# Optimization experiments

Hardware: AMD Instinct MI355X
Metric: run time of the kernel (lower is better)

## Reference

```python
import jax, jax.numpy as jnp
import numpy as np

N = 8192        # particles
NBH = 64        # black holes
L = 46.0        # box side -> ~32 neighbors per particle at radius 4.5
K = 4           # kernel_size per axis
KK = K * K * K
EXTENT = 9.0    # radius_scale(1.5) * 6 * particle_radius(1)
EXTENT_BH = 4.0 * EXTENT
EP = 300000     # padded particle-particle edge count
EB = 160000     # padded bh->particle edge count
CIN = 4         # vel(3) + mass(1)
C0, C1, C2, C3 = 32, 64, 64, 3
FOUR_OVER_PI = 4.0 / np.pi


def _ball_query_np(query, points, radius, cap, pad_seg):
    """Brute-force host-side ball query. Returns padded (src, dst); padding
    uses dst == pad_seg (a sentinel segment that is dropped later)."""
    r2 = radius * radius
    src, dst = [], []
    for i in range(0, query.shape[0], 1024):
        q = query[i:i + 1024]
        d2 = ((q[:, None, :] - points[None, :, :]) ** 2).sum(-1)
        m = (d2 < r2) & (d2 > 0.0)  # radius_search_ignore_query_points
        qi, pj = np.nonzero(m)
        dst.append(qi + i)
        src.append(pj)
    src = np.concatenate(src).astype(np.int32)
    dst = np.concatenate(dst).astype(np.int32)
    n = min(len(src), cap)
    out_s = np.zeros(cap, np.int32)
    out_d = np.full(cap, pad_seg, np.int32)
    out_s[:n] = src[:n]
    out_d[:n] = dst[:n]
    return out_s, out_d


def setup_inputs() -> dict:
    rng = np.random.RandomState(0)
    pos = (rng.rand(N, 3) * L).astype(np.float32)
    vel = rng.randn(N, 3).astype(np.float32)
    mass = rng.rand(N).astype(np.float32)
    bh_pos = (rng.rand(NBH, 3) * L).astype(np.float32)
    bh_vel = rng.randn(NBH, 3).astype(np.float32)
    bh_mass = (rng.rand(NBH) * 10.0).astype(np.float32)
    pp_src, pp_dst = _ball_query_np(pos, pos, EXTENT * 0.5, EP, N)
    bh_src, bh_dst = _ball_query_np(pos, bh_pos, EXTENT_BH * 0.5, EB, N)

    def w(*s):
        return (rng.randn(*s) * 0.05).astype(np.float32)

    inp = dict(
        pos=jnp.asarray(pos), vel=jnp.asarray(vel), mass=jnp.asarray(mass),
        bh_pos=jnp.asarray(bh_pos), bh_vel=jnp.asarray(bh_vel), bh_mass=jnp.asarray(bh_mass),
        pp_src=jnp.asarray(pp_src), pp_dst=jnp.asarray(pp_dst),
        bh_src=jnp.asarray(bh_src), bh_dst=jnp.asarray(bh_dst),
        W0a=jnp.asarray(w(K, K, K, CIN, C0)), b0a=jnp.zeros(C0, jnp.float32),
        Wd0=jnp.asarray(w(CIN, C0)), bd0=jnp.zeros(C0, jnp.float32),
        W0b=jnp.asarray(w(K, K, K, CIN, C0)), b0b=jnp.zeros(C0, jnp.float32),
        W1=jnp.asarray(w(K, K, K, 3 * C0, C1)), b1=jnp.zeros(C1, jnp.float32),
        Wd1=jnp.asarray(w(3 * C0, C1)), bd1=jnp.zeros(C1, jnp.float32),
        W2=jnp.asarray(w(K, K, K, C1, C2)), b2=jnp.zeros(C2, jnp.float32),
        Wd2=jnp.asarray(w(C1, C2)), bd2=jnp.zeros(C2, jnp.float32),
        W3=jnp.asarray(w(K, K, K, C2, C3)), b3=jnp.zeros(C3, jnp.float32),
        Wd3=jnp.asarray(w(C2, C3)), bd3=jnp.zeros(C3, jnp.float32),
    )
    return inp


def _ball_to_cube(p):
    """Volume-preserving map from unit ball to cube [-1,1]^3 (sphere->cylinder->cube)."""
    eps = 1e-8
    x, y, z = p[..., 0], p[..., 1], p[..., 2]
    sq = x * x + y * y + z * z
    nrm = jnp.sqrt(sq)
    xy = x * x + y * y
    # sphere -> cylinder
    caps = 1.25 * z * z > xy
    s_caps = jnp.sqrt(3.0 * nrm / (nrm + jnp.abs(z) + eps))
    s_side = nrm / jnp.sqrt(xy + eps)
    s = jnp.where(caps, s_caps, s_side)
    valid = sq > eps
    cx = jnp.where(valid, x * s, 0.0)
    cy = jnp.where(valid, y * s, 0.0)
    cz = jnp.where(valid, jnp.where(caps, jnp.sign(z) * nrm, 1.5 * z), 0.0)
    # cylinder -> cube (concentric disc-to-square, area preserving)
    rxy = jnp.sqrt(cx * cx + cy * cy)
    regA = cx * cx >= cy * cy
    safe_cx = jnp.where(jnp.abs(cx) > eps, cx, 1.0)
    safe_cy = jnp.where(jnp.abs(cy) > eps, cy, 1.0)
    uA = jnp.sign(cx) * rxy
    vA = uA * FOUR_OVER_PI * jnp.arctan(cy / safe_cx)
    vB = jnp.sign(cy) * rxy
    uB = vB * FOUR_OVER_PI * jnp.arctan(cx / safe_cy)
    okxy = rxy > eps
    u = jnp.where(okxy, jnp.where(regA, uA, uB), 0.0)
    v = jnp.where(okxy, jnp.where(regA, vA, vB), 0.0)
    return jnp.stack([u, v, cz], axis=-1)


def _cconv(feats, pos_src, pos_dst, src, dst, W, b, extent):
    """ContinuousConv: ball-query edges (src->dst), poly6 window, trilinear
    kernel interpolation (align_corners=True), scatter-sum, no normalization."""
    n_out = pos_dst.shape[0]
    radius = 0.5 * extent
    ps = jnp.take(pos_src, src, axis=0)                       # [E,3]
    pd = jnp.take(pos_dst, jnp.minimum(dst, n_out - 1), axis=0)
    d = (ps - pd) * (1.0 / radius)                            # normalized offsets
    r_sqr = jnp.sum(d * d, axis=-1)
    win = jnp.clip((1.0 - r_sqr) ** 3, 0.0, 1.0)              # window_poly6
    u = _ball_to_cube(d)                                      # in [-1,1]^3
    t = (u + 1.0) * (0.5 * (K - 1))                           # align_corners grid coords
    i0f = jnp.clip(jnp.floor(t), 0, K - 2)
    i0 = i0f.astype(jnp.int32)
    f = t - i0f                                               # trilinear fractions
    fe = jnp.take(feats, src, axis=0) * win[:, None]          # [E,Cin]
    Cin = feats.shape[1]
    Wf = W.reshape(KK, Cin, -1)
    T = jnp.zeros(((n_out + 1) * KK, Cin), feats.dtype)
    for dx in (0, 1):
        wx = f[:, 0] if dx else 1.0 - f[:, 0]
        for dy in (0, 1):
            wy = f[:, 1] if dy else 1.0 - f[:, 1]
            for dz in (0, 1):
                wz = f[:, 2] if dz else 1.0 - f[:, 2]
                k = ((i0[:, 0] + dx) * K + (i0[:, 1] + dy)) * K + (i0[:, 2] + dz)
                idx = dst * KK + k                            # sentinel dst==n_out dropped
                T = T + jax.ops.segment_sum((wx * wy * wz)[:, None] * fe, idx,
                                            num_segments=(n_out + 1) * KK)
    T = T.reshape(n_out + 1, KK, Cin)[:n_out]                 # [N,64,Cin]
    return jnp.einsum('nkc,kcd->nd', T, Wf) + b


def _forward(pos, vel, mass, bh_pos, bh_vel, bh_mass,
             W0a, b0a, Wd0, bd0, W0b, b0b, W1, b1, Wd1, bd1,
             W2, b2, Wd2, bd2, W3, b3, Wd3, bd3,
             pp_src, pp_dst, bh_src, bh_dst):
    feats = jnp.concatenate([vel, mass[:, None]], axis=-1)        # [N,4]
    bh_feats = jnp.concatenate([bh_vel, bh_mass[:, None]], axis=-1)
    c0 = _cconv(feats, pos, pos, pp_src, pp_dst, W0a, b0a, EXTENT)      # [N,32]
    d0 = feats @ Wd0 + bd0                                               # [N,32]
    cb = _cconv(bh_feats, bh_pos, pos, bh_src, bh_dst, W0b, b0b, EXTENT_BH)
    h = jnp.concatenate([c0, cb, d0], axis=-1)                           # [N,96]
    c1 = jax.nn.relu(_cconv(h, pos, pos, pp_src, pp_dst, W1, b1, EXTENT))
    d1 = jax.nn.relu(h @ Wd1 + bd1)
    h1 = c1 + d1                                                         # 64 != 96 -> no residual
    c2 = jax.nn.relu(_cconv(h1, pos, pos, pp_src, pp_dst, W2, b2, EXTENT))
    d2 = jax.nn.relu(h1 @ Wd2 + bd2)
    h2 = c2 + d2 + h1                                                    # 64 == 64 -> residual
    c3 = _cconv(h2, pos, pos, pp_src, pp_dst, W3, b3, EXTENT)
    d3 = h2 @ Wd3 + bd3
    return c3 + d3                                                       # accelerations [N,3]


def reference(pos, vel, mass, bh_pos, bh_vel, bh_mass,
              pp_src, pp_dst, bh_src, bh_dst,
              W0a, b0a, Wd0, bd0, W0b, b0b, W1, b1, Wd1, bd1,
              W2, b2, Wd2, bd2, W3, b3, Wd3, bd3):
    return _forward(pos, vel, mass, bh_pos, bh_vel, bh_mass,
                    W0a, b0a, Wd0, bd0, W0b, b0b, W1, b1, Wd1, bd1,
                    W2, b2, Wd2, bd2, W3, b3, Wd3, bd3,
                    pp_src, pp_dst, bh_src, bh_dst)
```

## Files before the change

kernel.cpp:

```cpp
#include <hip/hip_runtime.h>
#include <math.h>

#define NPART 8192
#define NBHX  64
#define EPX   300000
#define EBX   160000
#define FOUR_OVER_PI 1.27323954473516f

typedef __attribute__((ext_vector_type(8))) short bf16x8;
typedef __attribute__((ext_vector_type(4))) float f32x4;

__device__ __forceinline__ float signf(float x){ return (x>0.f)?1.f:((x<0.f)?-1.f:0.f); }
__device__ __forceinline__ unsigned short f2bf(float f){
  unsigned u = __float_as_uint(f);
  u += 0x7FFFu + ((u >> 16) & 1u);
  return (unsigned short)(u >> 16);
}
__device__ __forceinline__ float bf2f(unsigned short h){
  return __uint_as_float(((unsigned)h) << 16);
}
__device__ __forceinline__ float bfl(unsigned u){ return __uint_as_float(u << 16); }
__device__ __forceinline__ float bfh(unsigned u){ return __uint_as_float(u & 0xffff0000u); }

__global__ void feats_kernel(const float* __restrict__ vel, const float* __restrict__ mass,
                             const float* __restrict__ bhvel, const float* __restrict__ bhmass,
                             float* __restrict__ feats, float* __restrict__ bhfeats) {
  int i = blockIdx.x*256 + threadIdx.x;
  if (i < NPART) {
    feats[i*4+0]=vel[i*3+0]; feats[i*4+1]=vel[i*3+1]; feats[i*4+2]=vel[i*3+2]; feats[i*4+3]=mass[i];
  }
  if (i < NBHX) {
    bhfeats[i*4+0]=bhvel[i*3+0]; bhfeats[i*4+1]=bhvel[i*3+1]; bhfeats[i*4+2]=bhvel[i*3+2]; bhfeats[i*4+3]=bhmass[i];
  }
}

__global__ void geom_kernel(const float* __restrict__ ppos, const float* __restrict__ qpos,
                            const int* __restrict__ src, const int* __restrict__ dst,
                            int E, int n_out, float inv_radius,
                            int* __restrict__ gsrc, int* __restrict__ gbase, float* __restrict__ gw) {
  int e = blockIdx.x*256 + threadIdx.x;
  if (e >= E) return;
  int s = src[e], t = dst[e];
  gsrc[e] = s;
  if (t >= n_out) {
    gbase[e] = 0;
    for (int j=0;j<8;j++) gw[(size_t)e*8+j] = 0.f;
    return;
  }
  float x = (ppos[s*3+0] - qpos[t*3+0]) * inv_radius;
  float y = (ppos[s*3+1] - qpos[t*3+1]) * inv_radius;
  float z = (ppos[s*3+2] - qpos[t*3+2]) * inv_radius;
  float r2 = x*x + y*y + z*z;
  float w1 = 1.f - r2;
  float win = fminf(fmaxf(w1*w1*w1, 0.f), 1.f);
  const float eps = 1e-8f;
  float sq = r2;
  float nrm = sqrtf(sq);
  float xy = x*x + y*y;
  bool caps = (1.25f*z*z > xy);
  float s_caps = sqrtf(3.f*nrm/(nrm + fabsf(z) + eps));
  float s_side = nrm / sqrtf(xy + eps);
  float sc = caps ? s_caps : s_side;
  bool valid = sq > eps;
  float cx = valid ? x*sc : 0.f;
  float cy = valid ? y*sc : 0.f;
  float cz = valid ? (caps ? signf(z)*nrm : 1.5f*z) : 0.f;
  float rxy = sqrtf(cx*cx + cy*cy);
  bool regA = (cx*cx >= cy*cy);
  float safe_cx = (fabsf(cx) > eps) ? cx : 1.0f;
  float safe_cy = (fabsf(cy) > eps) ? cy : 1.0f;
  float uA = signf(cx)*rxy;
  float vA = uA * FOUR_OVER_PI * atanf(cy/safe_cx);
  float vB = signf(cy)*rxy;
  float uB = vB * FOUR_OVER_PI * atanf(cx/safe_cy);
  bool okxy = rxy > eps;
  float u = okxy ? (regA ? uA : uB) : 0.f;
  float v = okxy ? (regA ? vA : vB) : 0.f;
  float tt[3] = { (u+1.f)*1.5f, (v+1.f)*1.5f, (cz+1.f)*1.5f };
  int i0[3]; float f[3];
#pragma unroll
  for (int ax=0; ax<3; ax++) {
    float tf = floorf(tt[ax]);
    tf = fminf(fmaxf(tf, 0.f), 2.f);
    i0[ax] = (int)tf;
    f[ax] = tt[ax] - tf;
  }
  gbase[e] = (i0[0]*4 + i0[1])*4 + i0[2];
  float wx0 = 1.f - f[0], wx1 = f[0];
#pragma unroll
  for (int q=0;q<4;q++) {
    float wyz = win * ((q&2) ? f[1] : 1.f - f[1]) * ((q&1) ? f[2] : 1.f - f[2]);
    gw[(size_t)e*8 + q*2 + 0] = wyz * wx0;
    gw[(size_t)e*8 + q*2 + 1] = wyz * wx1;
  }
}

__global__ void csr_kernel(const int* __restrict__ dst, int E, int* __restrict__ rs) {
  int n = blockIdx.x*256 + threadIdx.x;
  if (n > NPART) return;
  int lo = 0, hi = E;
  while (lo < hi) { int mid = (lo+hi)>>1; if (dst[mid] < n) lo = mid+1; else hi = mid; }
  rs[n] = lo;
}

__global__ void zerohist_kernel(int* __restrict__ hist) {
  int i = blockIdx.x*256 + threadIdx.x;
  if (i < 4096) hist[i] = 0;
}
__global__ void cellhist_kernel(const float* __restrict__ pos, int* __restrict__ cell,
                                int* __restrict__ hist) {
  int i = blockIdx.x*256 + threadIdx.x;
  if (i >= NPART) return;
  const float inv = 16.0f/46.0f;
  int ix = min(15, max(0, (int)(pos[i*3+0]*inv)));
  int iy = min(15, max(0, (int)(pos[i*3+1]*inv)));
  int iz = min(15, max(0, (int)(pos[i*3+2]*inv)));
  int c = (ix*16+iy)*16+iz;
  cell[i] = c;
  atomicAdd(&hist[c], 1);
}
__global__ __launch_bounds__(256) void scan_kernel(const int* __restrict__ hist, int* __restrict__ offs) {
  __shared__ int wsum[4];
  int t = threadIdx.x;
  int base = t*16;
  int loc[16]; int s = 0;
#pragma unroll
  for (int i=0;i<16;i++){ loc[i]=s; s+=hist[base+i]; }
  int lane = t & 63, wv = t >> 6;
  int pre = s;
  for (int off=1; off<64; off<<=1) {
    int v = __shfl_up(pre, off);
    if (lane >= off) pre += v;
  }
  if (lane == 63) wsum[wv] = pre;
  __syncthreads();
  int wbase = 0;
  for (int w=0; w<wv; w++) wbase += wsum[w];
  int ex = wbase + pre - s;
#pragma unroll
  for (int i=0;i<16;i++) offs[base+i] = ex + loc[i];
}
__global__ void scatterorder_kernel(const int* __restrict__ cell, int* __restrict__ offs,
                                    int* __restrict__ order) {
  int i = blockIdx.x*256 + threadIdx.x;
  if (i >= NPART) return;
  int p = atomicAdd(&offs[cell[i]], 1);
  order[p] = i;
}

__device__ __forceinline__ int swz_block(int bid, int nb) {
  return (bid & 7)*(nb >> 3) + (bid >> 3);
}

__global__ void wtransY_kernel(const float* __restrict__ W, int KC, int CO, int DP,
                               unsigned short* __restrict__ BT) {
  int idx = blockIdx.x*256 + threadIdx.x;
  int N = 64*DP;
  if (idx >= N*KC) return;
  int n = idx / KC, c = idx - n*KC;
  int k = n / DP, d = n - k*DP;
  float v = (d < CO) ? W[((size_t)k*KC + c)*CO + d] : 0.f;
  BT[idx] = f2bf(v);
}

__global__ void y0_kernel(const float* __restrict__ feats4, const float* __restrict__ W0,
                          int NS, unsigned short* __restrict__ Y0) {
  int idx = blockIdx.x*256 + threadIdx.x;
  if (idx >= NS*256) return;
  int oct = idx & 3, k = (idx>>2) & 63, s = idx >> 8;
  float4 f = *(const float4*)(feats4 + (size_t)s*4);
  const float* w = W0 + (size_t)k*128 + oct*8;
  unsigned short o[8];
#pragma unroll
  for (int i=0;i<8;i++) {
    float v = f.x*w[i] + f.y*w[32+i] + f.z*w[64+i] + f.w*w[96+i];
    o[i] = f2bf(v);
  }
  uint4 u;
  u.x = (unsigned)o[0] | ((unsigned)o[1]<<16);
  u.y = (unsigned)o[2] | ((unsigned)o[3]<<16);
  u.z = (unsigned)o[4] | ((unsigned)o[5]<<16);
  u.w = (unsigned)o[6] | ((unsigned)o[7]<<16);
  *(uint4*)(Y0 + ((size_t)s*64 + k)*32 + oct*8) = u;
}

__global__ __launch_bounds__(256) void gemm_y_kernel(
    const unsigned short* __restrict__ A, const unsigned short* __restrict__ BT,
    int KC, int Ntot, unsigned short* __restrict__ Y) {
  const int wid  = threadIdx.x >> 6;
  const int lane = threadIdx.x & 63;
  const int r = lane & 15, g = lane >> 4;
  const int m0 = blockIdx.x*128 + wid*32;
  const int n0 = blockIdx.y*64;
  f32x4 acc[2][4];
#pragma unroll
  for (int h=0;h<2;h++)
#pragma unroll
    for (int n=0;n<4;n++) acc[h][n] = (f32x4){0.f,0.f,0.f,0.f};
  const unsigned short* A0 = A + (size_t)(m0 + r)*KC;
  const unsigned short* A1 = A + (size_t)(m0 + 16 + r)*KC;
  for (int k0 = 0; k0 < KC; k0 += 32) {
    int ko = k0 + g*8;
    bf16x8 a0 = *(const bf16x8*)(A0 + ko);
    bf16x8 a1 = *(const bf16x8*)(A1 + ko);
#pragma unroll
    for (int n=0; n<4; n++) {
      bf16x8 b = *(const bf16x8*)(BT + (size_t)(n0 + n*16 + r)*KC + ko);
      acc[0][n] = __builtin_amdgcn_mfma_f32_16x16x32_bf16(a0, b, acc[0][n], 0, 0, 0);
      acc[1][n] = __builtin_amdgcn_mfma_f32_16x16x32_bf16(a1, b, acc[1][n], 0, 0, 0);
    }
  }
#pragma unroll
  for (int h=0;h<2;h++)
#pragma unroll
    for (int n=0;n<4;n++)
#pragma unroll
      for (int j=0;j<4;j++)
        Y[(size_t)(m0 + h*16 + g*4 + j)*Ntot + n0 + n*16 + r] = f2bf(acc[h][n][j]);
}

__device__ __forceinline__ void xor_add4(f32x4& a, int mask) {
  a.x += __shfl_xor(a.x, mask);
  a.y += __shfl_xor(a.y, mask);
  a.z += __shfl_xor(a.z, mask);
  a.w += __shfl_xor(a.w, mask);
}

__global__ __launch_bounds__(256) void gather_l0_kernel(
    const int* __restrict__ order,
    const int* __restrict__ rsP, const int* __restrict__ gsP, const int* __restrict__ gbP, const float* __restrict__ gwP,
    const int* __restrict__ rsB, const int* __restrict__ gsB, const int* __restrict__ gbB, const float* __restrict__ gwB,
    const unsigned short* __restrict__ Y0a, const unsigned short* __restrict__ Y0b,
    const float* __restrict__ feats4, const float* __restrict__ Wd0, const float* __restrict__ bd0,
    const float* __restrict__ b0a, const float* __restrict__ b0b,
    float* __restrict__ hf, unsigned short* __restrict__ hb) {
  const int sb = swz_block(blockIdx.x, gridDim.x);
  const int node = order[sb*4 + (threadIdx.x >> 6)];
  const int lane = threadIdx.x & 63;
  const int j = lane >> 3, cg = lane & 7;
  const int koff = ((j&4)<<2) | ((j&2)<<1) | (j&1);
  const int widx = (j&3)*2 + (j>>2);
  f32x4 accP = {0.f,0.f,0.f,0.f}, accB = {0.f,0.f,0.f,0.f};
  {
    int e0 = rsP[node], e1 = rsP[node+1];
    int e = e0;
    for (; e + 4 <= e1; e += 4) {
      uint2 y[4]; float w[4];
#pragma unroll
      for (int i=0;i<4;i++) {
        int s = gsP[e+i], b = gbP[e+i];
        y[i] = *(const uint2*)(Y0a + ((size_t)(s*64 + b + koff))*32 + cg*4);
        w[i] = gwP[(size_t)(e+i)*8 + widx];
      }
#pragma unroll
      for (int i=0;i<4;i++) {
        accP.x += w[i]*bfl(y[i].x); accP.y += w[i]*bfh(y[i].x);
        accP.z += w[i]*bfl(y[i].y); accP.w += w[i]*bfh(y[i].y);
      }
    }
    for (; e < e1; e++) {
      int s = gsP[e], b = gbP[e];
      uint2 y = *(const uint2*)(Y0a + ((size_t)(s*64 + b + koff))*32 + cg*4);
      float w = gwP[(size_t)e*8 + widx];
      accP.x += w*bfl(y.x); accP.y += w*bfh(y.x);
      accP.z += w*bfl(y.y); accP.w += w*bfh(y.y);
    }
  }
  {
    int e0 = rsB[node], e1 = rsB[node+1];
    int e = e0;
    for (; e + 4 <= e1; e += 4) {
      uint2 y[4]; float w[4];
#pragma unroll
      for (int i=0;i<4;i++) {
        int s = gsB[e+i], b = gbB[e+i];
        y[i] = *(const uint2*)(Y0b + ((size_t)(s*64 + b + koff))*32 + cg*4);
        w[i] = gwB[(size_t)(e+i)*8 + widx];
      }
#pragma unroll
      for (int i=0;i<4;i++) {
        accB.x += w[i]*bfl(y[i].x); accB.y += w[i]*bfh(y[i].x);
        accB.z += w[i]*bfl(y[i].y); accB.w += w[i]*bfh(y[i].y);
      }
    }
    for (; e < e1; e++) {
      int s = gsB[e], b = gbB[e];
      uint2 y = *(const uint2*)(Y0b + ((size_t)(s*64 + b + koff))*32 + cg*4);
      float w = gwB[(size_t)e*8 + widx];
      accB.x += w*bfl(y.x); accB.y += w*bfh(y.x);
      accB.z += w*bfl(y.y); accB.w += w*bfh(y.y);
    }
  }
  xor_add4(accP, 8);  xor_add4(accP, 16); xor_add4(accP, 32);
  xor_add4(accB, 8);  xor_add4(accB, 16); xor_add4(accB, 32);
  if (lane < 8) {
    float4 f = *(const float4*)(feats4 + (size_t)node*4);
    float4 ba = *(const float4*)(b0a + cg*4);
    float4 bb = *(const float4*)(b0b + cg*4);
    float4 bdv = *(const float4*)(bd0 + cg*4);
    float4 w0v = *(const float4*)(Wd0 + 0*32 + cg*4);
    float4 w1v = *(const float4*)(Wd0 + 1*32 + cg*4);
    float4 w2v = *(const float4*)(Wd0 + 2*32 + cg*4);
    float4 w3v = *(const float4*)(Wd0 + 3*32 + cg*4);
    float4 dd;
    dd.x = bdv.x + f.x*w0v.x + f.y*w1v.x + f.z*w2v.x + f.w*w3v.x;
    dd.y = bdv.y + f.x*w0v.y + f.y*w1v.y + f.z*w2v.y + f.w*w3v.y;
    dd.z = bdv.z + f.x*w0v.z + f.y*w1v.z + f.z*w2v.z + f.w*w3v.z;
    dd.w = bdv.w + f.x*w0v.w + f.y*w1v.w + f.z*w2v.w + f.w*w3v.w;
    float4 c0; c0.x = accP.x + ba.x; c0.y = accP.y + ba.y; c0.z = accP.z + ba.z; c0.w = accP.w + ba.w;
    float4 cb; cb.x = accB.x + bb.x; cb.y = accB.y + bb.y; cb.z = accB.z + bb.z; cb.w = accB.w + bb.w;
    size_t o = (size_t)node*96;
    *(float4*)(hf + o + cg*4)      = c0;
    *(float4*)(hf + o + 32 + cg*4) = cb;
    *(float4*)(hf + o + 64 + cg*4) = dd;
    ushort4 u0 = {f2bf(c0.x), f2bf(c0.y), f2bf(c0.z), f2bf(c0.w)};
    ushort4 u1 = {f2bf(cb.x), f2bf(cb.y), f2bf(cb.z), f2bf(cb.w)};
    ushort4 u2 = {f2bf(dd.x), f2bf(dd.y), f2bf(dd.z), f2bf(dd.w)};
    *(ushort4*)(hb + o + cg*4)      = u0;
    *(ushort4*)(hb + o + 32 + cg*4) = u1;
    *(ushort4*)(hb + o + 64 + cg*4) = u2;
  }
}

template<int DCIN, bool ADDSKIP>
__global__ __launch_bounds__(128) void gather64_kernel(
    const int* __restrict__ order,
    const int* __restrict__ rs, const int* __restrict__ gsrc, const int* __restrict__ gbase,
    const float* __restrict__ gw, const unsigned short* __restrict__ Y,
    const float* __restrict__ Xf, const float* __restrict__ Wd, const float* __restrict__ bd,
    const float* __restrict__ bconv, const float* __restrict__ skip,
    float* __restrict__ outf, unsigned short* __restrict__ outb) {
  const int sb = swz_block(blockIdx.x, gridDim.x);
  const int node = order[sb];
  const int wave = threadIdx.x >> 6;
  const int lane = threadIdx.x & 63;
  const int q = lane >> 4, cl = lane & 15;
  const int koffA = ((q&2)<<1) | (q&1);
  __shared__ __align__(16) float red[64*4];
  f32x4 acc = {0.f,0.f,0.f,0.f};
  const int e0 = rs[node], e1 = rs[node+1];
  int e = e0 + wave;
  for (; e + 6 < e1; e += 8) {
    uint2 lo[4], hi[4]; float2 w[4];
#pragma unroll
    for (int i=0;i<4;i++) {
      int ee = e + i*2;
      int s = gsrc[ee], b = gbase[ee];
      const unsigned short* p = Y + ((size_t)(s*64 + b + koffA))*64 + cl*4;
      lo[i] = *(const uint2*)p;
      hi[i] = *(const uint2*)(p + 1024);
      w[i]  = *(const float2*)(gw + (size_t)ee*8 + q*2);
    }
#pragma unroll
    for (int i=0;i<4;i++) {
      acc.x += w[i].x*bfl(lo[i].x) + w[i].y*bfl(hi[i].x);
      acc.y += w[i].x*bfh(lo[i].x) + w[i].y*bfh(hi[i].x);
      acc.z += w[i].x*bfl(lo[i].y) + w[i].y*bfl(hi[i].y);
      acc.w += w[i].x*bfh(lo[i].y) + w[i].y*bfh(hi[i].y);
    }
  }
  for (; e < e1; e += 2) {
    int s = gsrc[e], b = gbase[e];
    const unsigned short* p = Y + ((size_t)(s*64 + b + koffA))*64 + cl*4;
    uint2 lo = *(const uint2*)p;
    uint2 hi = *(const uint2*)(p + 1024);
    float2 w = *(const float2*)(gw + (size_t)e*8 + q*2);
    acc.x += w.x*bfl(lo.x) + w.y*bfl(hi.x);
    acc.y += w.x*bfh(lo.x) + w.y*bfh(hi.x);
    acc.z += w.x*bfl(lo.y) + w.y*bfl(hi.y);
    acc.w += w.x*bfh(lo.y) + w.y*bfh(hi.y);
  }
  if (wave == 1) {
    *(f32x4*)(red + lane*4) = acc;
  }
  __syncthreads();
  if (wave == 0) {
    f32x4 o = *(const f32x4*)(red + lane*4);
    acc.x += o.x; acc.y += o.y; acc.z += o.z; acc.w += o.w;
    constexpr int KQ = DCIN/4;
    f32x4 dd = {0.f,0.f,0.f,0.f};
    const float* x = Xf + (size_t)node*DCIN + q*KQ;
#pragma unroll 8
    for (int kk=0; kk<KQ; kk++) {
      float xv = x[kk];
      float4 wv = *(const float4*)(Wd + (size_t)(q*KQ+kk)*64 + cl*4);
      dd.x += xv*wv.x; dd.y += xv*wv.y; dd.z += xv*wv.z; dd.w += xv*wv.w;
    }
    xor_add4(acc, 16); xor_add4(acc, 32);
    xor_add4(dd, 16);  xor_add4(dd, 32);
    if (lane < 16) {
      float4 bc = *(const float4*)(bconv + cl*4);
      float4 bdv = *(const float4*)(bd + cl*4);
      float4 v;
      v.x = fmaxf(acc.x + bc.x, 0.f) + fmaxf(dd.x + bdv.x, 0.f);
      v.y = fmaxf(acc.y + bc.y, 0.f) + fmaxf(dd.y + bdv.y, 0.f);
      v.z = fmaxf(acc.z + bc.z, 0.f) + fmaxf(dd.z + bdv.z, 0.f);
      v.w = fmaxf(acc.w + bc.w, 0.f) + fmaxf(dd.w + bdv.w, 0.f);
      if (ADDSKIP) {
        float4 sk = *(const float4*)(skip + (size_t)node*64 + cl*4);
        v.x += sk.x; v.y += sk.y; v.z += sk.z; v.w += sk.w;
      }
      *(float4*)(outf + (size_t)node*64 + cl*4) = v;
      ushort4 u = {f2bf(v.x), f2bf(v.y), f2bf(v.z), f2bf(v.w)};
      *(ushort4*)(outb + (size_t)node*64 + cl*4) = u;
    }
  }
}

__global__ __launch_bounds__(256) void gather3_kernel(
    const int* __restrict__ order,
    const int* __restrict__ rs, const int* __restrict__ gsrc, const int* __restrict__ gbase,
    const float* __restrict__ gw, const unsigned short* __restrict__ Y3,
    const float* __restrict__ h2f, const float* __restrict__ Wd3, const float* __restrict__ bd3,
    const float* __restrict__ b3, float* __restrict__ out) {
  const int sb = swz_block(blockIdx.x, gridDim.x);
  const int node = order[sb*4 + (threadIdx.x >> 6)];
  const int lane = threadIdx.x & 63;
  const int e2 = lane >> 5, j = (lane >> 2) & 7, dd = lane & 3;
  const int koff = ((j&4)<<2)|((j&2)<<1)|(j&1);
  const int widx = (j&3)*2 + (j>>2);
  float acc = 0.f;
  const int e0 = rs[node], e1 = rs[node+1];
  for (int e = e0; e < e1; e += 2) {
    int ee = e + e2;
    bool v = ee < e1;
    int ix = v ? ee : e;
    int s = gsrc[ix], base = gbase[ix];
    float w = v ? gw[(size_t)ix*8 + widx] : 0.f;
    acc += w * bf2f(Y3[((size_t)s*64 + base + koff)*4 + dd]);
  }
  acc += __shfl_xor(acc, 4);
  acc += __shfl_xor(acc, 8);
  acc += __shfl_xor(acc, 16);
  acc += __shfl_down(acc, 32);
  if (lane < 3) {
    float d3 = bd3[lane];
    const float* x = h2f + (size_t)node*64;
#pragma unroll 8
    for (int c=0;c<64;c++) d3 += x[c]*Wd3[c*3 + lane];
    out[(size_t)node*3 + lane] = acc + b3[lane] + d3;
  }
}

extern "C" void kernel_launch(void* const* d_in, const int* in_sizes, int n_in,
                              void* d_out, int out_size, void* d_ws, size_t ws_size,
                              hipStream_t stream) {
  const float* pos    = (const float*)d_in[0];
  const float* vel    = (const float*)d_in[1];
  const float* mass   = (const float*)d_in[2];
  const float* bh_pos = (const float*)d_in[3];
  const float* bh_vel = (const float*)d_in[4];
  const float* bh_mass= (const float*)d_in[5];
  const int* pp_src   = (const int*)d_in[6];
  const int* pp_dst   = (const int*)d_in[7];
  const int* bh_src   = (const int*)d_in[8];
  const int* bh_dst   = (const int*)d_in[9];
  const float* W0a=(const float*)d_in[10]; const float* b0a=(const float*)d_in[11];
  const float* Wd0=(const float*)d_in[12]; const float* bd0=(const float*)d_in[13];
  const float* W0b=(const float*)d_in[14]; const float* b0b=(const float*)d_in[15];
  const float* W1 =(const float*)d_in[16]; const float* b1 =(const float*)d_in[17];
  const float* Wd1=(const float*)d_in[18]; const float* bd1=(const float*)d_in[19];
  const float* W2 =(const float*)d_in[20]; const float* b2 =(const float*)d_in[21];
  const float* Wd2=(const float*)d_in[22]; const float* bd2=(const float*)d_in[23];
  const float* W3 =(const float*)d_in[24]; const float* b3 =(const float*)d_in[25];
  const float* Wd3=(const float*)d_in[26]; const float* bd3=(const float*)d_in[27];
  float* out = (float*)d_out;
  char* wsb = (char*)d_ws;

  size_t off = 0;
  auto alloc = [&](size_t nbytes){ size_t o = off; off += (nbytes + 255) & ~((size_t)255); return o; };
  size_t feats_o   = alloc((size_t)NPART*4*4);
  size_t bhfeats_o = alloc((size_t)NBHX*4*4);
  size_t rs_pp_o   = alloc(8256*4);
  size_t rs_bh_o   = alloc(8256*4);
  size_t gsrc_pp_o = alloc((size_t)EPX*4);
  size_t gbase_pp_o= alloc((size_t)EPX*4);
  size_t gw_pp_o   = alloc((size_t)EPX*8*4);
  size_t gsrc_bh_o = alloc((size_t)EBX*4);
  size_t gbase_bh_o= alloc((size_t)EBX*4);
  size_t gw_bh_o   = alloc((size_t)EBX*8*4);
  size_t hf_o  = alloc((size_t)NPART*96*4);
  size_t hb_o  = alloc((size_t)NPART*96*2);
  size_t h1f_o = alloc((size_t)NPART*64*4);
  size_t h1b_o = alloc((size_t)NPART*64*2);
  size_t h2f_o = alloc((size_t)NPART*64*4);
  size_t h2b_o = alloc((size_t)NPART*64*2);
  size_t bt1_o = alloc((size_t)4096*96*2);
  size_t bt2_o = alloc((size_t)4096*64*2);
  size_t bt3_o = alloc((size_t)256*64*2);
  size_t y0b_o = alloc((size_t)NBHX*64*32*2);
  size_t cell_o = alloc((size_t)NPART*4);
  size_t hist_o = alloc((size_t)4096*4);
  size_t order_o= alloc((size_t)NPART*4);
  size_t y_o   = alloc((size_t)NPART*4096*2);

  float* featsP = (float*)(wsb + feats_o); float* bhfeatsP = (float*)(wsb + bhfeats_o);
  int* rsPP = (int*)(wsb + rs_pp_o); int* rsBH = (int*)(wsb + rs_bh_o);
  int* gsP = (int*)(wsb + gsrc_pp_o); int* gbP = (int*)(wsb + gbase_pp_o); float* gwP = (float*)(wsb + gw_pp_o);
  int* gsB = (int*)(wsb + gsrc_bh_o); int* gbB = (int*)(wsb + gbase_bh_o); float* gwB = (float*)(wsb + gw_bh_o);
  float* hf  = (float*)(wsb + hf_o);  unsigned short* hb  = (unsigned short*)(wsb + hb_o);
  float* h1f = (float*)(wsb + h1f_o); unsigned short* h1b = (unsigned short*)(wsb + h1b_o);
  float* h2f = (float*)(wsb + h2f_o); unsigned short* h2b = (unsigned short*)(wsb + h2b_o);
  unsigned short* BT1 = (unsigned short*)(wsb + bt1_o);
  unsigned short* BT2 = (unsigned short*)(wsb + bt2_o);
  unsigned short* BT3 = (unsigned short*)(wsb + bt3_o);
  unsigned short* Y0b = (unsigned short*)(wsb + y0b_o);
  int* cellA = (int*)(wsb + cell_o);
  int* histA = (int*)(wsb + hist_o);
  int* orderA= (int*)(wsb + order_o);
  unsigned short* Ybuf = (unsigned short*)(wsb + y_o);

  feats_kernel<<<(NPART+255)/256, 256, 0, stream>>>(vel, mass, bh_vel, bh_mass, featsP, bhfeatsP);
  geom_kernel<<<(EPX+255)/256, 256, 0, stream>>>(pos, pos, pp_src, pp_dst, EPX, NPART, 1.f/4.5f, gsP, gbP, gwP);
  geom_kernel<<<(EBX+255)/256, 256, 0, stream>>>(bh_pos, pos, bh_src, bh_dst, EBX, NPART, 1.f/18.f, gsB, gbB, gwB);
  csr_kernel<<<(NPART+1+255)/256, 256, 0, stream>>>(pp_dst, EPX, rsPP);
  csr_kernel<<<(NPART+1+255)/256, 256, 0, stream>>>(bh_dst, EBX, rsBH);
  zerohist_kernel<<<16, 256, 0, stream>>>(histA);
  cellhist_kernel<<<NPART/256, 256, 0, stream>>>(pos, cellA, histA);
  scan_kernel<<<1, 256, 0, stream>>>(histA, histA);
  scatterorder_kernel<<<NPART/256, 256, 0, stream>>>(cellA, histA, orderA);
  wtransY_kernel<<<((size_t)4096*96+255)/256, 256, 0, stream>>>(W1, 96, 64, 64, BT1);
  wtransY_kernel<<<((size_t)4096*64+255)/256, 256, 0, stream>>>(W2, 64, 64, 64, BT2);
  wtransY_kernel<<<((size_t)256*64+255)/256, 256, 0, stream>>>(W3, 64, 3, 4, BT3);

  y0_kernel<<<(NPART*256+255)/256, 256, 0, stream>>>(featsP, W0a, NPART, Ybuf);
  y0_kernel<<<(NBHX*256+255)/256, 256, 0, stream>>>(bhfeatsP, W0b, NBHX, Y0b);
  gather_l0_kernel<<<NPART/4, 256, 0, stream>>>(orderA, rsPP, gsP, gbP, gwP, rsBH, gsB, gbB, gwB,
                                                Ybuf, Y0b, featsP, Wd0, bd0, b0a, b0b, hf, hb);
  {
    dim3 g(NPART/128, 4096/64);
    gemm_y_kernel<<<g, 256, 0, stream>>>(hb, BT1, 96, 4096, Ybuf);
    gather64_kernel<96,false><<<NPART, 128, 0, stream>>>(orderA, rsPP, gsP, gbP, gwP, Ybuf,
        hf, Wd1, bd1, b1, nullptr, h1f, h1b);
  }
  {
    dim3 g(NPART/128, 4096/64);
    gemm_y_kernel<<<g, 256, 0, stream>>>(h1b, BT2, 64, 4096, Ybuf);
    gather64_kernel<64,true><<<NPART, 128, 0, stream>>>(orderA, rsPP, gsP, gbP, gwP, Ybuf,
        h1f, Wd2, bd2, b2, h1f, h2f, h2b);
  }
  {
    dim3 g(NPART/128, 256/64);
    gemm_y_kernel<<<g, 256, 0, stream>>>(h2b, BT3, 64, 256, Ybuf);
    gather3_kernel<<<NPART/4, 256, 0, stream>>>(orderA, rsPP, gsP, gbP, gwP, Ybuf,
        h2f, Wd3, bd3, b3, out);
  }
}
```

Baseline: 248.9 us.

## Merge setup kernels, pack src/base index, remap gather64 lanes to 8 corners

Several small setup launches are fused: hist zeroing goes into feats_kernel, the two CSR searches into one kernel, the three weight transposes into one, and the two y0 launches into one. The geometry pass now stores a single premultiplied src*64+base index and weights in natural corner order, so each gather does one index load instead of two. gather64 is remapped so each lane handles one of 8 corners with 16-byte loads of 8 channels, replacing two 8-byte loads per lane. This adds a wider shuffle reduction and more shared memory in exchange.

Result: faster. 214.8 us (-13.7%).

```diff
diff --git a/kernel.cpp b/kernel.cpp
--- a/kernel.cpp
+++ b/kernel.cpp
@@ -24,7 +24,8 @@
 
 __global__ void feats_kernel(const float* __restrict__ vel, const float* __restrict__ mass,
                              const float* __restrict__ bhvel, const float* __restrict__ bhmass,
-                             float* __restrict__ feats, float* __restrict__ bhfeats) {
+                             float* __restrict__ feats, float* __restrict__ bhfeats,
+                             int* __restrict__ hist) {
   int i = blockIdx.x*256 + threadIdx.x;
   if (i < NPART) {
     feats[i*4+0]=vel[i*3+0]; feats[i*4+1]=vel[i*3+1]; feats[i*4+2]=vel[i*3+2]; feats[i*4+3]=mass[i];
@@ -32,18 +33,18 @@
   if (i < NBHX) {
     bhfeats[i*4+0]=bhvel[i*3+0]; bhfeats[i*4+1]=bhvel[i*3+1]; bhfeats[i*4+2]=bhvel[i*3+2]; bhfeats[i*4+3]=bhmass[i];
   }
+  if (i < 4096) hist[i] = 0;
 }
 
 __global__ void geom_kernel(const float* __restrict__ ppos, const float* __restrict__ qpos,
                             const int* __restrict__ src, const int* __restrict__ dst,
                             int E, int n_out, float inv_radius,
-                            int* __restrict__ gsrc, int* __restrict__ gbase, float* __restrict__ gw) {
+                            int* __restrict__ gsb, float* __restrict__ gw) {
   int e = blockIdx.x*256 + threadIdx.x;
   if (e >= E) return;
   int s = src[e], t = dst[e];
-  gsrc[e] = s;
   if (t >= n_out) {
-    gbase[e] = 0;
+    gsb[e] = s*64;
     for (int j=0;j<8;j++) gw[(size_t)e*8+j] = 0.f;
     return;
   }
@@ -54,14 +55,13 @@
   float w1 = 1.f - r2;
   float win = fminf(fmaxf(w1*w1*w1, 0.f), 1.f);
   const float eps = 1e-8f;
-  float sq = r2;
-  float nrm = sqrtf(sq);
+  float nrm = sqrtf(r2);
   float xy = x*x + y*y;
   bool caps = (1.25f*z*z > xy);
   float s_caps = sqrtf(3.f*nrm/(nrm + fabsf(z) + eps));
   float s_side = nrm / sqrtf(xy + eps);
   float sc = caps ? s_caps : s_side;
-  bool valid = sq > eps;
+  bool valid = r2 > eps;
   float cx = valid ? x*sc : 0.f;
   float cy = valid ? y*sc : 0.f;
   float cz = valid ? (caps ? signf(z)*nrm : 1.5f*z) : 0.f;
@@ -85,28 +85,32 @@
     i0[ax] = (int)tf;
     f[ax] = tt[ax] - tf;
   }
-  gbase[e] = (i0[0]*4 + i0[1])*4 + i0[2];
-  float wx0 = 1.f - f[0], wx1 = f[0];
-#pragma unroll
-  for (int q=0;q<4;q++) {
-    float wyz = win * ((q&2) ? f[1] : 1.f - f[1]) * ((q&1) ? f[2] : 1.f - f[2]);
-    gw[(size_t)e*8 + q*2 + 0] = wyz * wx0;
-    gw[(size_t)e*8 + q*2 + 1] = wyz * wx1;
-  }
-}
-
-__global__ void csr_kernel(const int* __restrict__ dst, int E, int* __restrict__ rs) {
-  int n = blockIdx.x*256 + threadIdx.x;
-  if (n > NPART) return;
-  int lo = 0, hi = E;
-  while (lo < hi) { int mid = (lo+hi)>>1; if (dst[mid] < n) lo = mid+1; else hi = mid; }
-  rs[n] = lo;
-}
-
-__global__ void zerohist_kernel(int* __restrict__ hist) {
+  gsb[e] = s*64 + ((i0[0]*4 + i0[1])*4 + i0[2]);
+#pragma unroll
+  for (int j=0;j<8;j++) {
+    float wx = (j&4) ? f[0] : 1.f - f[0];
+    float wy = (j&2) ? f[1] : 1.f - f[1];
+    float wz = (j&1) ? f[2] : 1.f - f[2];
+    gw[(size_t)e*8+j] = win * wx * wy * wz;
+  }
+}
+
+__global__ void csr2_kernel(const int* __restrict__ dstP, const int* __restrict__ dstB,
+                            int* __restrict__ rsP, int* __restrict__ rsB) {
   int i = blockIdx.x*256 + threadIdx.x;
-  if (i < 4096) hist[i] = 0;
-}
+  if (i <= NPART) {
+    int lo = 0, hi = EPX;
+    while (lo < hi) { int mid = (lo+hi)>>1; if (dstP[mid] < i) lo = mid+1; else hi = mid; }
+    rsP[i] = lo;
+  }
+  int k = i - (NPART+1);
+  if (k >= 0 && k <= NPART) {
+    int lo = 0, hi = EBX;
+    while (lo < hi) { int mid = (lo+hi)>>1; if (dstB[mid] < k) lo = mid+1; else hi = mid; }
+    rsB[k] = lo;
+  }
+}
+
 __global__ void cellhist_kernel(const float* __restrict__ pos, int* __restrict__ cell,
                                 int* __restrict__ hist) {
   int i = blockIdx.x*256 + threadIdx.x;
@@ -152,23 +156,36 @@
   return (bid & 7)*(nb >> 3) + (bid >> 3);
 }
 
-__global__ void wtransY_kernel(const float* __restrict__ W, int KC, int CO, int DP,
-                               unsigned short* __restrict__ BT) {
+__global__ void wtrans3_kernel(const float* __restrict__ W1, const float* __restrict__ W2,
+                               const float* __restrict__ W3,
+                               unsigned short* __restrict__ BT1, unsigned short* __restrict__ BT2,
+                               unsigned short* __restrict__ BT3) {
   int idx = blockIdx.x*256 + threadIdx.x;
-  int N = 64*DP;
-  if (idx >= N*KC) return;
-  int n = idx / KC, c = idx - n*KC;
-  int k = n / DP, d = n - k*DP;
-  float v = (d < CO) ? W[((size_t)k*KC + c)*CO + d] : 0.f;
-  BT[idx] = f2bf(v);
-}
-
-__global__ void y0_kernel(const float* __restrict__ feats4, const float* __restrict__ W0,
-                          int NS, unsigned short* __restrict__ Y0) {
+  const int S1 = 4096*96, S2 = 4096*64, S3 = 256*64;
+  if (idx < S1) {
+    int n = idx/96, c = idx - n*96; int k = n>>6, d = n&63;
+    BT1[idx] = f2bf(W1[((size_t)k*96 + c)*64 + d]);
+  } else if (idx < S1+S2) {
+    int t = idx - S1; int n = t>>6, c = t&63; int k = n>>6, d = n&63;
+    BT2[t] = f2bf(W2[((size_t)k*64 + c)*64 + d]);
+  } else if (idx < S1+S2+S3) {
+    int t = idx - S1 - S2; int n = t>>6, c = t&63; int k = n>>2, d = n&3;
+    BT3[t] = f2bf((d < 3) ? W3[((size_t)k*64 + c)*3 + d] : 0.f);
+  }
+}
+
+__global__ void y0_kernel(const float* __restrict__ feats4, const float* __restrict__ bhfeats,
+                          const float* __restrict__ W0a, const float* __restrict__ W0b,
+                          unsigned short* __restrict__ Y0a, unsigned short* __restrict__ Y0b) {
   int idx = blockIdx.x*256 + threadIdx.x;
-  if (idx >= NS*256) return;
+  if (idx >= (NPART+NBHX)*256) return;
   int oct = idx & 3, k = (idx>>2) & 63, s = idx >> 8;
-  float4 f = *(const float4*)(feats4 + (size_t)s*4);
+  bool bh = (s >= NPART);
+  int sl = bh ? s - NPART : s;
+  const float* fp = (bh ? bhfeats : feats4) + (size_t)sl*4;
+  const float* W0 = bh ? W0b : W0a;
+  unsigned short* Y = (bh ? Y0b : Y0a) + ((size_t)sl*64 + k)*32 + oct*8;
+  float4 f = *(const float4*)fp;
   const float* w = W0 + (size_t)k*128 + oct*8;
   unsigned short o[8];
 #pragma unroll
@@ -181,7 +198,7 @@
   u.y = (unsigned)o[2] | ((unsigned)o[3]<<16);
   u.z = (unsigned)o[4] | ((unsigned)o[5]<<16);
   u.w = (unsigned)o[6] | ((unsigned)o[7]<<16);
-  *(uint4*)(Y0 + ((size_t)s*64 + k)*32 + oct*8) = u;
+  *(uint4*)Y = u;
 }
 
 __global__ __launch_bounds__(256) void gemm_y_kernel(
@@ -228,18 +245,17 @@
 
 __global__ __launch_bounds__(256) void gather_l0_kernel(
     const int* __restrict__ order,
-    const int* __restrict__ rsP, const int* __restrict__ gsP, const int* __restrict__ gbP, const float* __restrict__ gwP,
-    const int* __restrict__ rsB, const int* __restrict__ gsB, const int* __restrict__ gbB, const float* __restrict__ gwB,
+    const int* __restrict__ rsP, const int* __restrict__ gsbP, const float* __restrict__ gwP,
+    const int* __restrict__ rsB, const int* __restrict__ gsbB, const float* __restrict__ gwB,
     const unsigned short* __restrict__ Y0a, const unsigned short* __restrict__ Y0b,
     const float* __restrict__ feats4, const float* __restrict__ Wd0, const float* __restrict__ bd0,
     const float* __restrict__ b0a, const float* __restrict__ b0b,
     float* __restrict__ hf, unsigned short* __restrict__ hb) {
-  const int sb = swz_block(blockIdx.x, gridDim.x);
-  const int node = order[sb*4 + (threadIdx.x >> 6)];
+  const int sw = swz_block(blockIdx.x, gridDim.x);
+  const int node = order[sw*4 + (threadIdx.x >> 6)];
   const int lane = threadIdx.x & 63;
   const int j = lane >> 3, cg = lane & 7;
   const int koff = ((j&4)<<2) | ((j&2)<<1) | (j&1);
-  const int widx = (j&3)*2 + (j>>2);
   f32x4 accP = {0.f,0.f,0.f,0.f}, accB = {0.f,0.f,0.f,0.f};
   {
     int e0 = rsP[node], e1 = rsP[node+1];
@@ -248,9 +264,9 @@
       uint2 y[4]; float w[4];
 #pragma unroll
       for (int i=0;i<4;i++) {
-        int s = gsP[e+i], b = gbP[e+i];
-        y[i] = *(const uint2*)(Y0a + ((size_t)(s*64 + b + koff))*32 + cg*4);
-        w[i] = gwP[(size_t)(e+i)*8 + widx];
+        int sb = gsbP[e+i];
+        y[i] = *(const uint2*)(Y0a + ((size_t)(sb + koff))*32 + cg*4);
+        w[i] = gwP[(size_t)(e+i)*8 + j];
       }
 #pragma unroll
       for (int i=0;i<4;i++) {
@@ -259,9 +275,9 @@
       }
     }
     for (; e < e1; e++) {
-      int s = gsP[e], b = gbP[e];
-      uint2 y = *(const uint2*)(Y0a + ((size_t)(s*64 + b + koff))*32 + cg*4);
-      float w = gwP[(size_t)e*8 + widx];
+      int sb = gsbP[e];
+      uint2 y = *(const uint2*)(Y0a + ((size_t)(sb + koff))*32 + cg*4);
+      float w = gwP[(size_t)e*8 + j];
       accP.x += w*bfl(y.x); accP.y += w*bfh(y.x);
       accP.z += w*bfl(y.y); accP.w += w*bfh(y.y);
     }
@@ -273,9 +289,9 @@
       uint2 y[4]; float w[4];
 #pragma unroll
       for (int i=0;i<4;i++) {
-        int s = gsB[e+i], b = gbB[e+i];
-        y[i] = *(const uint2*)(Y0b + ((size_t)(s*64 + b + koff))*32 + cg*4);
-        w[i] = gwB[(size_t)(e+i)*8 + widx];
+        int sb = gsbB[e+i];
+        y[i] = *(const uint2*)(Y0b + ((size_t)(sb + koff))*32 + cg*4);
+        w[i] = gwB[(size_t)(e+i)*8 + j];
       }
 #pragma unroll
       for (int i=0;i<4;i++) {
@@ -284,9 +300,9 @@
       }
     }
     for (; e < e1; e++) {
-      int s = gsB[e], b = gbB[e];
-      uint2 y = *(const uint2*)(Y0b + ((size_t)(s*64 + b + koff))*32 + cg*4);
-      float w = gwB[(size_t)e*8 + widx];
+      int sb = gsbB[e];
+      uint2 y = *(const uint2*)(Y0b + ((size_t)(sb + koff))*32 + cg*4);
+      float w = gwB[(size_t)e*8 + j];
       accB.x += w*bfl(y.x); accB.y += w*bfh(y.x);
       accB.z += w*bfl(y.y); accB.w += w*bfh(y.y);
     }
@@ -325,109 +341,124 @@
 template<int DCIN, bool ADDSKIP>
 __global__ __launch_bounds__(128) void gather64_kernel(
     const int* __restrict__ order,
-    const int* __restrict__ rs, const int* __restrict__ gsrc, const int* __restrict__ gbase,
-    const float* __restrict__ gw, const unsigned short* __restrict__ Y,
+    const int* __restrict__ rs, const int* __restrict__ gsb, const float* __restrict__ gw,
+    const unsigned short* __restrict__ Y,
     const float* __restrict__ Xf, const float* __restrict__ Wd, const float* __restrict__ bd,
     const float* __restrict__ bconv, const float* __restrict__ skip,
     float* __restrict__ outf, unsigned short* __restrict__ outb) {
-  const int sb = swz_block(blockIdx.x, gridDim.x);
-  const int node = order[sb];
+  const int sw = swz_block(blockIdx.x, gridDim.x);
+  const int node = order[sw];
   const int wave = threadIdx.x >> 6;
   const int lane = threadIdx.x & 63;
-  const int q = lane >> 4, cl = lane & 15;
-  const int koffA = ((q&2)<<1) | (q&1);
-  __shared__ __align__(16) float red[64*4];
-  f32x4 acc = {0.f,0.f,0.f,0.f};
+  const int j = lane >> 3, cg = lane & 7;
+  const int koff = ((j&4)<<2) | ((j&2)<<1) | (j&1);
+  __shared__ __align__(16) float red[64*8];
+  f32x4 accA = {0.f,0.f,0.f,0.f}, accB = {0.f,0.f,0.f,0.f};
   const int e0 = rs[node], e1 = rs[node+1];
   int e = e0 + wave;
   for (; e + 6 < e1; e += 8) {
-    uint2 lo[4], hi[4]; float2 w[4];
+    uint4 y[4]; float w[4];
 #pragma unroll
     for (int i=0;i<4;i++) {
       int ee = e + i*2;
-      int s = gsrc[ee], b = gbase[ee];
-      const unsigned short* p = Y + ((size_t)(s*64 + b + koffA))*64 + cl*4;
-      lo[i] = *(const uint2*)p;
-      hi[i] = *(const uint2*)(p + 1024);
-      w[i]  = *(const float2*)(gw + (size_t)ee*8 + q*2);
+      int sb = gsb[ee];
+      y[i] = *(const uint4*)(Y + ((size_t)(sb + koff))*64 + cg*8);
+      w[i] = gw[(size_t)ee*8 + j];
     }
 #pragma unroll
     for (int i=0;i<4;i++) {
-      acc.x += w[i].x*bfl(lo[i].x) + w[i].y*bfl(hi[i].x);
-      acc.y += w[i].x*bfh(lo[i].x) + w[i].y*bfh(hi[i].x);
-      acc.z += w[i].x*bfl(lo[i].y) + w[i].y*bfl(hi[i].y);
-      acc.w += w[i].x*bfh(lo[i].y) + w[i].y*bfh(hi[i].y);
+      accA.x += w[i]*bfl(y[i].x); accA.y += w[i]*bfh(y[i].x);
+      accA.z += w[i]*bfl(y[i].y); accA.w += w[i]*bfh(y[i].y);
+      accB.x += w[i]*bfl(y[i].z); accB.y += w[i]*bfh(y[i].z);
+      accB.z += w[i]*bfl(y[i].w); accB.w += w[i]*bfh(y[i].w);
     }
   }
   for (; e < e1; e += 2) {
-    int s = gsrc[e], b = gbase[e];
-    const unsigned short* p = Y + ((size_t)(s*64 + b + koffA))*64 + cl*4;
-    uint2 lo = *(const uint2*)p;
-    uint2 hi = *(const uint2*)(p + 1024);
-    float2 w = *(const float2*)(gw + (size_t)e*8 + q*2);
-    acc.x += w.x*bfl(lo.x) + w.y*bfl(hi.x);
-    acc.y += w.x*bfh(lo.x) + w.y*bfh(hi.x);
-    acc.z += w.x*bfl(lo.y) + w.y*bfl(hi.y);
-    acc.w += w.x*bfh(lo.y) + w.y*bfh(hi.y);
+    int sb = gsb[e];
+    uint4 y = *(const uint4*)(Y + ((size_t)(sb + koff))*64 + cg*8);
+    float w = gw[(size_t)e*8 + j];
+    accA.x += w*bfl(y.x); accA.y += w*bfh(y.x);
+    accA.z += w*bfl(y.y); accA.w += w*bfh(y.y);
+    accB.x += w*bfl(y.z); accB.y += w*bfh(y.z);
+    accB.z += w*bfl(y.w); accB.w += w*bfh(y.w);
   }
   if (wave == 1) {
-    *(f32x4*)(red + lane*4) = acc;
+    *(f32x4*)(red + lane*8)     = accA;
+    *(f32x4*)(red + lane*8 + 4) = accB;
   }
   __syncthreads();
   if (wave == 0) {
-    f32x4 o = *(const f32x4*)(red + lane*4);
-    acc.x += o.x; acc.y += o.y; acc.z += o.z; acc.w += o.w;
-    constexpr int KQ = DCIN/4;
-    f32x4 dd = {0.f,0.f,0.f,0.f};
-    const float* x = Xf + (size_t)node*DCIN + q*KQ;
-#pragma unroll 8
+    {
+      f32x4 oA = *(const f32x4*)(red + lane*8);
+      f32x4 oB = *(const f32x4*)(red + lane*8 + 4);
+      accA.x += oA.x; accA.y += oA.y; accA.z += oA.z; accA.w += oA.w;
+      accB.x += oB.x; accB.y += oB.y; accB.z += oB.z; accB.w += oB.w;
+    }
+    constexpr int KQ = DCIN/8;
+    f32x4 ddA = {0.f,0.f,0.f,0.f}, ddB = {0.f,0.f,0.f,0.f};
+    const float* x = Xf + (size_t)node*DCIN + j*KQ;
+#pragma unroll
     for (int kk=0; kk<KQ; kk++) {
       float xv = x[kk];
-      float4 wv = *(const float4*)(Wd + (size_t)(q*KQ+kk)*64 + cl*4);
-      dd.x += xv*wv.x; dd.y += xv*wv.y; dd.z += xv*wv.z; dd.w += xv*wv.w;
-    }
-    xor_add4(acc, 16); xor_add4(acc, 32);
-    xor_add4(dd, 16);  xor_add4(dd, 32);
-    if (lane < 16) {
-      float4 bc = *(const float4*)(bconv + cl*4);
-      float4 bdv = *(const float4*)(bd + cl*4);
-      float4 v;
-      v.x = fmaxf(acc.x + bc.x, 0.f) + fmaxf(dd.x + bdv.x, 0.f);
-      v.y = fmaxf(acc.y + bc.y, 0.f) + fmaxf(dd.y + bdv.y, 0.f);
-      v.z = fmaxf(acc.z + bc.z, 0.f) + fmaxf(dd.z + bdv.z, 0.f);
-      v.w = fmaxf(acc.w + bc.w, 0.f) + fmaxf(dd.w + bdv.w, 0.f);
+      float4 w0 = *(const float4*)(Wd + (size_t)(j*KQ+kk)*64 + cg*8);
+      float4 w1 = *(const float4*)(Wd + (size_t)(j*KQ+kk)*64 + cg*8 + 4);
+      ddA.x += xv*w0.x; ddA.y += xv*w0.y; ddA.z += xv*w0.z; ddA.w += xv*w0.w;
+      ddB.x += xv*w1.x; ddB.y += xv*w1.y; ddB.z += xv*w1.z; ddB.w += xv*w1.w;
+    }
+    xor_add4(accA, 8); xor_add4(accA, 16); xor_add4(accA, 32);
+    xor_add4(accB, 8); xor_add4(accB, 16); xor_add4(accB, 32);
+    xor_add4(ddA, 8);  xor_add4(ddA, 16);  xor_add4(ddA, 32);
+    xor_add4(ddB, 8);  xor_add4(ddB, 16);  xor_add4(ddB, 32);
+    if (lane < 8) {
+      float4 bc0 = *(const float4*)(bconv + cg*8);
+      float4 bc1 = *(const float4*)(bconv + cg*8 + 4);
+      float4 bd0v = *(const float4*)(bd + cg*8);
+      float4 bd1v = *(const float4*)(bd + cg*8 + 4);
+      float4 v0, v1;
+      v0.x = fmaxf(accA.x + bc0.x, 0.f) + fmaxf(ddA.x + bd0v.x, 0.f);
+      v0.y = fmaxf(accA.y + bc0.y, 0.f) + fmaxf(ddA.y + bd0v.y, 0.f);
+      v0.z = fmaxf(accA.z + bc0.z, 0.f) + fmaxf(ddA.z + bd0v.z, 0.f);
+      v0.w = fmaxf(accA.w + bc0.w, 0.f) + fmaxf(ddA.w + bd0v.w, 0.f);
+      v1.x = fmaxf(accB.x + bc1.x, 0.f) + fmaxf(ddB.x + bd1v.x, 0.f);
+      v1.y = fmaxf(accB.y + bc1.y, 0.f) + fmaxf(ddB.y + bd1v.y, 0.f);
+      v1.z = fmaxf(accB.z + bc1.z, 0.f) + fmaxf(ddB.z + bd1v.z, 0.f);
+      v1.w = fmaxf(accB.w + bc1.w, 0.f) + fmaxf(ddB.w + bd1v.w, 0.f);
       if (ADDSKIP) {
-        float4 sk = *(const float4*)(skip + (size_t)node*64 + cl*4);
-        v.x += sk.x; v.y += sk.y; v.z += sk.z; v.w += sk.w;
+        float4 s0 = *(const float4*)(skip + (size_t)node*64 + cg*8);
+        float4 s1 = *(const float4*)(skip + (size_t)node*64 + cg*8 + 4);
+        v0.x += s0.x; v0.y += s0.y; v0.z += s0.z; v0.w += s0.w;
+        v1.x += s1.x; v1.y += s1.y; v1.z += s1.z; v1.w += s1.w;
       }
-      *(float4*)(outf + (size_t)node*64 + cl*4) = v;
-      ushort4 u = {f2bf(v.x), f2bf(v.y), f2bf(v.z), f2bf(v.w)};
-      *(ushort4*)(outb + (size_t)node*64 + cl*4) = u;
+      *(float4*)(outf + (size_t)node*64 + cg*8)     = v0;
+      *(float4*)(outf + (size_t)node*64 + cg*8 + 4) = v1;
+      ushort4 u0 = {f2bf(v0.x), f2bf(v0.y), f2bf(v0.z), f2bf(v0.w)};
+      ushort4 u1 = {f2bf(v1.x), f2bf(v1.y), f2bf(v1.z), f2bf(v1.w)};
+      *(ushort4*)(outb + (size_t)node*64 + cg*8)     = u0;
+      *(ushort4*)(outb + (size_t)node*64 + cg*8 + 4) = u1;
     }
   }
 }
 
 __global__ __launch_bounds__(256) void gather3_kernel(
     const int* __restrict__ order,
-    const int* __restrict__ rs, const int* __restrict__ gsrc, const int* __restrict__ gbase,
-    const float* __restrict__ gw, const unsigned short* __restrict__ Y3,
+    const int* __restrict__ rs, const int* __restrict__ gsb, const float* __restrict__ gw,
+    const unsigned short* __restrict__ Y3,
     const float* __restrict__ h2f, const float* __restrict__ Wd3, const float* __restrict__ bd3,
     const float* __restrict__ b3, float* __restrict__ out) {
-  const int sb = swz_block(blockIdx.x, gridDim.x);
-  const int node = order[sb*4 + (threadIdx.x >> 6)];
+  const int sw = swz_block(blockIdx.x, gridDim.x);
+  const int node = order[sw*4 + (threadIdx.x >> 6)];
   const int lane = threadIdx.x & 63;
   const int e2 = lane >> 5, j = (lane >> 2) & 7, dd = lane & 3;
   const int koff = ((j&4)<<2)|((j&2)<<1)|(j&1);
-  const int widx = (j&3)*2 + (j>>2);
   float acc = 0.f;
   const int e0 = rs[node], e1 = rs[node+1];
   for (int e = e0; e < e1; e += 2) {
     int ee = e + e2;
     bool v = ee < e1;
     int ix = v ? ee : e;
-    int s = gsrc[ix], base = gbase[ix];
-    float w = v ? gw[(size_t)ix*8 + widx] : 0.f;
-    acc += w * bf2f(Y3[((size_t)s*64 + base + koff)*4 + dd]);
+    int sb = gsb[ix];
+    float w = v ? gw[(size_t)ix*8 + j] : 0.f;
+    acc += w * bf2f(Y3[((size_t)(sb + koff))*4 + dd]);
   }
   acc += __shfl_xor(acc, 4);
   acc += __shfl_xor(acc, 8);
@@ -473,11 +504,9 @@
   size_t bhfeats_o = alloc((size_t)NBHX*4*4);
   size_t rs_pp_o   = alloc(8256*4);
   size_t rs_bh_o   = alloc(8256*4);
-  size_t gsrc_pp_o = alloc((size_t)EPX*4);
-  size_t gbase_pp_o= alloc((size_t)EPX*4);
+  size_t gsb_pp_o  = alloc((size_t)EPX*4);
   size_t gw_pp_o   = alloc((size_t)EPX*8*4);
-  size_t gsrc_bh_o = alloc((size_t)EBX*4);
-  size_t gbase_bh_o= alloc((size_t)EBX*4);
+  size_t gsb_bh_o  = alloc((size_t)EBX*4);
   size_t gw_bh_o   = alloc((size_t)EBX*8*4);
   size_t hf_o  = alloc((size_t)NPART*96*4);
   size_t hb_o  = alloc((size_t)NPART*96*2);
@@ -496,8 +525,8 @@
 
   float* featsP = (float*)(wsb + feats_o); float* bhfeatsP = (float*)(wsb + bhfeats_o);
   int* rsPP = (int*)(wsb + rs_pp_o); int* rsBH = (int*)(wsb + rs_bh_o);
-  int* gsP = (int*)(wsb + gsrc_pp_o); int* gbP = (int*)(wsb + gbase_pp_o); float* gwP = (float*)(wsb + gw_pp_o);
-  int* gsB = (int*)(wsb + gsrc_bh_o); int* gbB = (int*)(wsb + gbase_bh_o); float* gwB = (float*)(wsb + gw_bh_o);
+  int* gsbP = (int*)(wsb + gsb_pp_o); float* gwP = (float*)(wsb + gw_pp_o);
+  int* gsbB = (int*)(wsb + gsb_bh_o); float* gwB = (float*)(wsb + gw_bh_o);
   float* hf  = (float*)(wsb + hf_o);  unsigned short* hb  = (unsigned short*)(wsb + hb_o);
   float* h1f = (float*)(wsb + h1f_o); unsigned short* h1b = (unsigned short*)(wsb + h1b_o);
   float* h2f = (float*)(wsb + h2f_o); unsigned short* h2b = (unsigned short*)(wsb + h2b_o);
@@ -510,39 +539,34 @@
   int* orderA= (int*)(wsb + order_o);
   unsigned short* Ybuf = (unsigned short*)(wsb + y_o);
 
-  feats_kernel<<<(NPART+255)/256, 256, 0, stream>>>(vel, mass, bh_vel, bh_mass, featsP, bhfeatsP);
-  geom_kernel<<<(EPX+255)/256, 256, 0, stream>>>(pos, pos, pp_src, pp_dst, EPX, NPART, 1.f/4.5f, gsP, gbP, gwP);
-  geom_kernel<<<(EBX+255)/256, 256, 0, stream>>>(bh_pos, pos, bh_src, bh_dst, EBX, NPART, 1.f/18.f, gsB, gbB, gwB);
-  csr_kernel<<<(NPART+1+255)/256, 256, 0, stream>>>(pp_dst, EPX, rsPP);
-  csr_kernel<<<(NPART+1+255)/256, 256, 0, stream>>>(bh_dst, EBX, rsBH);
-  zerohist_kernel<<<16, 256, 0, stream>>>(histA);
+  feats_kernel<<<(NPART+255)/256, 256, 0, stream>>>(vel, mass, bh_vel, bh_mass, featsP, bhfeatsP, histA);
+  geom_kernel<<<(EPX+255)/256, 256, 0, stream>>>(pos, pos, pp_src, pp_dst, EPX, NPART, 1.f/4.5f, gsbP, gwP);
+  geom_kernel<<<(EBX+255)/256, 256, 0, stream>>>(bh_pos, pos, bh_src, bh_dst, EBX, NPART, 1.f/18.f, gsbB, gwB);
+  csr2_kernel<<<(2*(NPART+1)+255)/256, 256, 0, stream>>>(pp_dst, bh_dst, rsPP, rsBH);
   cellhist_kernel<<<NPART/256, 256, 0, stream>>>(pos, cellA, histA);
   scan_kernel<<<1, 256, 0, stream>>>(histA, histA);
   scatterorder_kernel<<<NPART/256, 256, 0, stream>>>(cellA, histA, orderA);
-  wtransY_kernel<<<((size_t)4096*96+255)/256, 256, 0, stream>>>(W1, 96, 64, 64, BT1);
-  wtransY_kernel<<<((size_t)4096*64+255)/256, 256, 0, stream>>>(W2, 64, 64, 64, BT2);
-  wtransY_kernel<<<((size_t)256*64+255)/256, 256, 0, stream>>>(W3, 64, 3, 4, BT3);
-
-  y0_kernel<<<(NPART*256+255)/256, 256, 0, stream>>>(featsP, W0a, NPART, Ybuf);
-  y0_kernel<<<(NBHX*256+255)/256, 256, 0, stream>>>(bhfeatsP, W0b, NBHX, Y0b);
-  gather_l0_kernel<<<NPART/4, 256, 0, stream>>>(orderA, rsPP, gsP, gbP, gwP, rsBH, gsB, gbB, gwB,
+  wtrans3_kernel<<<(4096*96 + 4096*64 + 256*64 + 255)/256, 256, 0, stream>>>(W1, W2, W3, BT1, BT2, BT3);
+
+  y0_kernel<<<((NPART+NBHX)*256+255)/256, 256, 0, stream>>>(featsP, bhfeatsP, W0a, W0b, Ybuf, Y0b);
+  gather_l0_kernel<<<NPART/4, 256, 0, stream>>>(orderA, rsPP, gsbP, gwP, rsBH, gsbB, gwB,
                                                 Ybuf, Y0b, featsP, Wd0, bd0, b0a, b0b, hf, hb);
   {
     dim3 g(NPART/128, 4096/64);
     gemm_y_kernel<<<g, 256, 0, stream>>>(hb, BT1, 96, 4096, Ybuf);
-    gather64_kernel<96,false><<<NPART, 128, 0, stream>>>(orderA, rsPP, gsP, gbP, gwP, Ybuf,
+    gather64_kernel<96,false><<<NPART, 128, 0, stream>>>(orderA, rsPP, gsbP, gwP, Ybuf,
         hf, Wd1, bd1, b1, nullptr, h1f, h1b);
   }
   {
     dim3 g(NPART/128, 4096/64);
     gemm_y_kernel<<<g, 256, 0, stream>>>(h1b, BT2, 64, 4096, Ybuf);
-    gather64_kernel<64,true><<<NPART, 128, 0, stream>>>(orderA, rsPP, gsP, gbP, gwP, Ybuf,
+    gather64_kernel<64,true><<<NPART, 128, 0, stream>>>(orderA, rsPP, gsbP, gwP, Ybuf,
         h1f, Wd2, bd2, b2, h1f, h2f, h2b);
   }
   {
     dim3 g(NPART/128, 256/64);
     gemm_y_kernel<<<g, 256, 0, stream>>>(h2b, BT3, 64, 256, Ybuf);
-    gather3_kernel<<<NPART/4, 256, 0, stream>>>(orderA, rsPP, gsP, gbP, gwP, Ybuf,
+    gather3_kernel<<<NPART/4, 256, 0, stream>>>(orderA, rsPP, gsbP, gwP, Ybuf,
         h2f, Wd3, bd3, b3, out);
   }
 }
```
